# Optimization experiments

Hardware: AMD Instinct MI355X
Metric: run time of the kernel (lower is better)

The kernel has to match this reference:

```python
import jax, jax.numpy as jnp
import numpy as np

W, BHS, SEQ, H = 8, 2, 1024, 2048
FFN_PER = (4 * H) // W  # per-partition 4h width = 1024

def setup_inputs() -> dict:
    key = jax.random.key(0)
    k1, k2, k3 = jax.random.split(key, 3)
    # xavier-normal-ish scale for weights
    s1 = (2.0 / (H + FFN_PER)) ** 0.5
    s2 = (2.0 / (FFN_PER + H)) ** 0.5
    return {
        "hidden_states": jax.random.normal(k1, (W, BHS, SEQ, H), dtype=jnp.float32),
        "w1": jax.random.normal(k2, (W, H, FFN_PER), dtype=jnp.float32) * s1,
        "b1": jnp.zeros((W, 1, FFN_PER), dtype=jnp.float32),
        "w2": jax.random.normal(k3, (W, FFN_PER, H), dtype=jnp.float32) * s2,
        "b2": jnp.zeros((W, H), dtype=jnp.float32),
        "idx_list": jnp.arange(W, dtype=jnp.int64),
    }

def reference(hidden_states, w1, b1, w2, b2, idx_list):
    w, bhs, seq, h = hidden_states.shape
    # view [W, bhs, seq, h] -> [W, bhs*seq, h]
    x = hidden_states.reshape(w, bhs * seq, h)
    # column-parallel: baddbmm(bias, x, w1) -> [W, N, 4h/W]
    inter = jnp.einsum('wnh,whf->wnf', x, w1) + b1
    # exact (erf) gelu, matching torch F.gelu default
    inter = jax.nn.gelu(inter, approximate=False)
    # row-parallel: baddbmm(bias, inter, w2) -> [W, N, h]
    out_bias = b2[:, None, :]  # [W, 1, out]
    out = jnp.einsum('wnf,wfo->wno', inter, w2) + out_bias
    return (out, out_bias)
```

## Files before the change

### kernel.cpp

```cpp
#include <hip/hip_runtime.h>
#include <hip/hip_bf16.h>
#include <math.h>


typedef float f32x4 __attribute__((ext_vector_type(4)));
typedef short bf16x8 __attribute__((ext_vector_type(8)));
typedef short bf16x4 __attribute__((ext_vector_type(4)));
typedef unsigned short u16;

#define NW 8
#define MDIM 2048
#define HDIM 2048
#define FFN  1024

static __device__ __forceinline__ u16 f32_to_bf16_rn(float f) {
  union { float f; unsigned u; } v; v.f = f;
  unsigned r = v.u + 0x7FFF + ((v.u >> 16) & 1);
  return (u16)(r >> 16);
}

static __device__ __forceinline__ void gload_lds16(const void* g, void* l) {
  __builtin_amdgcn_global_load_lds(
      (const __attribute__((address_space(1))) void*)g,
      (__attribute__((address_space(3))) void*)l, 16, 0, 0);
}

__global__ void convert_bf16_kernel(const float* __restrict__ in,
                                    u16* __restrict__ out,
                                    const float* __restrict__ b2,
                                    float* __restrict__ outb) {
  int bid = blockIdx.x;
  if (bid >= NW * MDIM * HDIM / 4 / 256) {
    int i = (bid - NW * MDIM * HDIM / 4 / 256) * 256 + threadIdx.x;
    if (i < NW * HDIM) outb[i] = b2[i];
    return;
  }
  size_t i = (size_t)bid * blockDim.x + threadIdx.x;
  f32x4 v = ((const f32x4*)in)[i];
  bf16x4 p;
  p[0] = (short)f32_to_bf16_rn(v.x);
  p[1] = (short)f32_to_bf16_rn(v.y);
  p[2] = (short)f32_to_bf16_rn(v.z);
  p[3] = (short)f32_to_bf16_rn(v.w);
  ((bf16x4*)out)[i] = p;
}

__global__ void convert_transpose_kernel(const float* __restrict__ in,
                                         u16* __restrict__ out, int R, int C) {
  __shared__ u16 tile[64][68];
  int w = blockIdx.z;
  int c0 = blockIdx.x * 64, r0 = blockIdx.y * 64;
  int t = threadIdx.x;
  const float* ip = in + (size_t)w * R * C;
  u16* op = out + (size_t)w * C * R;
  int tr = t >> 4;
  int tc4 = (t & 15) * 4;
#pragma unroll
  for (int j = 0; j < 4; ++j) {
    int r = tr + j * 16;
    f32x4 v = *(const f32x4*)(ip + (size_t)(r0 + r) * C + c0 + tc4);
    tile[r][tc4 + 0] = f32_to_bf16_rn(v.x);
    tile[r][tc4 + 1] = f32_to_bf16_rn(v.y);
    tile[r][tc4 + 2] = f32_to_bf16_rn(v.z);
    tile[r][tc4 + 3] = f32_to_bf16_rn(v.w);
  }
  __syncthreads();
#pragma unroll
  for (int j = 0; j < 4; ++j) {
    int c = tr + j * 16;
    bf16x4 p;
    p[0] = (short)tile[tc4 + 0][c];
    p[1] = (short)tile[tc4 + 1][c];
    p[2] = (short)tile[tc4 + 2][c];
    p[3] = (short)tile[tc4 + 3][c];
    *(bf16x4*)(op + (size_t)(c0 + c) * R + r0 + tc4) = p;
  }
}

#define STAGE_AH(dst, tt, h)                                                  \
  do {                                                                        \
    gload_lds16(gA + (size_t)(h) * 128 * rowK + (size_t)(tt) * 128,           \
                (dst) + (h) * 16384 + tid * 16);                              \
    gload_lds16(gA + ((size_t)(h) * 128 + 64) * rowK + (size_t)(tt) * 128,    \
                (dst) + (h) * 16384 + 8192 + tid * 16);                       \
  } while (0)
#define STAGE_BH(dst, tt, h)                                                  \
  do {                                                                        \
    gload_lds16(gB + (size_t)(h) * 128 * rowK + (size_t)(tt) * 128,           \
                (dst) + 32768 + (h) * 16384 + tid * 16);                      \
    gload_lds16(gB + ((size_t)(h) * 128 + 64) * rowK + (size_t)(tt) * 128,    \
                (dst) + 32768 + (h) * 16384 + 8192 + tid * 16);               \
  } while (0)

#define LOAD_A(DST, SB, q)                                                    \
  _Pragma("unroll") for (int ii = 0; ii < 2; ++ii)                            \
      _Pragma("unroll") for (int kk = 0; kk < 2; ++kk)                        \
          DST[ii][kk] = *(const bf16x8*)((SB) + Aoff +                        \
              ((q)*32 + ii * 16 + ra) * 128 + (colsw ^ (kk << 6)))
#define LOAD_B(DST, SB)                                                       \
  _Pragma("unroll") for (int jj = 0; jj < 4; ++jj)                            \
      _Pragma("unroll") for (int kk = 0; kk < 2; ++kk)                        \
          DST[jj][kk] = *(const bf16x8*)((SB) + Boff +                        \
              (brow + jj * 16 + ra) * 128 + (colsw ^ (kk << 6)))

#define DO_PHASE(q, AF, BF, STAGES, VMCODE, PREFETCH)                         \
  {                                                                           \
    STAGES;                                                                   \
    __builtin_amdgcn_s_barrier();                                             \
    asm volatile("s_waitcnt lgkmcnt(0)" ::: "memory");                        \
    __builtin_amdgcn_sched_barrier(0);                                        \
    __builtin_amdgcn_s_setprio(1);                                            \
    _Pragma("unroll") for (int ii = 0; ii < 2; ++ii)                          \
        _Pragma("unroll") for (int jj = 0; jj < 4; ++jj)                      \
            _Pragma("unroll") for (int kk = 0; kk < 2; ++kk)                  \
                acc[(q)*2 + ii][jj] =                                         \
                    __builtin_amdgcn_mfma_f32_16x16x32_bf16(                  \
                        AF[ii][kk], BF[jj][kk], acc[(q)*2 + ii][jj],          \
                        0, 0, 0);                                             \
    __builtin_amdgcn_s_setprio(0);                                            \
    VMCODE;                                                                   \
    PREFETCH;                                                                 \
    __builtin_amdgcn_sched_barrier(0);                                        \
  }

template <bool GELU, bool C_F32>
__global__ __launch_bounds__(512, 2) void mlp_gemm(
    const u16* __restrict__ A, const u16* __restrict__ Bt,
    const float* __restrict__ bias, void* __restrict__ Cptr,
    int M, int N, int K, int nN) {
  __shared__ __align__(16) char lds[131072];
  char* cur = lds;
  char* nxt = lds + 65536;

  const int bid = blockIdx.x;
  const int w = bid & 7;
  const int jb = bid >> 3;
  const int m0 = (jb / nN) * 256;
  const int n0 = (jb % nN) * 256;

  const int tid = threadIdx.x;
  const int wid = tid >> 6, lane = tid & 63;
  const int wr = wid >> 2, wc = wid & 3;
  const int qa = lane >> 4, ra = lane & 15;

  const u16* ap = A + (size_t)w * M * K;
  const u16* btp = Bt + (size_t)w * N * K;
  const float* bp = bias + (size_t)w * N;

  const size_t rowK = (size_t)K * 2;
  const int r8 = tid >> 3;
  const int csw = ((tid & 7) * 16) ^ ((r8 & 7) << 4);
  const char* gA = (const char*)ap + (size_t)(m0 + r8) * rowK + csw;
  const char* gB = (const char*)btp + (size_t)(n0 + r8) * rowK + csw;

  const int colsw = (qa * 16) ^ ((ra & 7) << 4);
  const int Aoff = wr * 16384;
  const int Boff = 32768 + (wc >> 1) * 16384;
  const int brow = (wc & 1) * 64;

  f32x4 acc[8][4];
#pragma unroll
  for (int i = 0; i < 8; ++i)
#pragma unroll
    for (int j = 0; j < 4; ++j)
#pragma unroll
      for (int r = 0; r < 4; ++r) acc[i][j][r] = 0.0f;

  const int NT = K >> 6;
  const int nIter = NT >> 1;

  STAGE_BH(cur, 0, 0); STAGE_BH(cur, 0, 1);
  STAGE_AH(cur, 0, 0); STAGE_AH(cur, 0, 1);
  STAGE_BH(nxt, 1, 0); STAGE_BH(nxt, 1, 1);
  asm volatile("s_waitcnt vmcnt(4)" ::: "memory");
  __builtin_amdgcn_sched_barrier(0);
  __builtin_amdgcn_s_barrier();

  bf16x8 afrA[2][2], afrB[2][2], bfrA[4][2], bfrB[4][2];
  LOAD_B(bfrA, cur);
  LOAD_A(afrA, cur, 0);
  __builtin_amdgcn_sched_barrier(0);

  for (int it = 0; it < nIter; ++it) {
    const int t = it * 2;
    const bool s2 = (t + 2) < NT;

    DO_PHASE(0, afrA, bfrA, { STAGE_AH(nxt, t + 1, 0); }, {},
             { LOAD_A(afrB, cur, 1); });
    DO_PHASE(1, afrB, bfrA,
             { STAGE_AH(nxt, t + 1, 1); if (s2) STAGE_BH(cur, t + 2, 0); }, {},
             { LOAD_A(afrA, cur, 2); });
    DO_PHASE(2, afrA, bfrA, { if (s2) STAGE_BH(cur, t + 2, 1); }, {
      if (s2) asm volatile("s_waitcnt vmcnt(4)" ::: "memory");
      else    asm volatile("s_waitcnt vmcnt(0)" ::: "memory");
      __builtin_amdgcn_sched_barrier(0);
    }, { LOAD_A(afrB, cur, 3); });
    DO_PHASE(3, afrB, bfrA, {}, {},
             { LOAD_B(bfrB, nxt); LOAD_A(afrA, nxt, 0); });

    DO_PHASE(0, afrA, bfrB, { if (s2) STAGE_AH(cur, t + 2, 0); }, {},
             { LOAD_A(afrB, nxt, 1); });
    DO_PHASE(1, afrB, bfrB,
             { if (s2) { STAGE_AH(cur, t + 2, 1); STAGE_BH(nxt, t + 3, 0); } }, {},
             { LOAD_A(afrA, nxt, 2); });
    DO_PHASE(2, afrA, bfrB, { if (s2) STAGE_BH(nxt, t + 3, 1); }, {
      if (s2) asm volatile("s_waitcnt vmcnt(4)" ::: "memory");
      else    asm volatile("s_waitcnt vmcnt(0)" ::: "memory");
      __builtin_amdgcn_sched_barrier(0);
    }, { LOAD_A(afrB, nxt, 3); });
    DO_PHASE(3, afrB, bfrB, {}, {},
             { LOAD_B(bfrA, cur); LOAD_A(afrA, cur, 0); });
  }

#pragma unroll
  for (int i = 0; i < 8; ++i) {
#pragma unroll
    for (int j = 0; j < 4; ++j) {
      int col = n0 + wc * 64 + j * 16 + ra;
      float bv = bp[col];
#pragma unroll
      for (int r = 0; r < 4; ++r) {
        int row = m0 + wr * 128 + i * 16 + qa * 4 + r;
        float v = acc[i][j][r] + bv;
        if (GELU) v = 0.5f * v * (1.0f + erff(v * 0.70710678118654752f));
        if (C_F32)
          ((float*)Cptr)[(size_t)w * M * N + (size_t)row * N + col] = v;
        else
          ((u16*)Cptr)[(size_t)w * M * N + (size_t)row * N + col] =
              f32_to_bf16_rn(v);
      }
    }
  }
}

extern "C" void kernel_launch(void* const* d_in, const int* in_sizes, int n_in,
                              void* d_out, int out_size, void* d_ws,
                              size_t ws_size, hipStream_t stream) {
  const float* hs = (const float*)d_in[0];
  const float* w1 = (const float*)d_in[1];
  const float* b1 = (const float*)d_in[2];
  const float* w2 = (const float*)d_in[3];
  const float* b2 = (const float*)d_in[4];

  u16* W1t = (u16*)d_ws;
  u16* W2t = W1t + (size_t)NW * FFN * HDIM;
  u16* inter = W2t + (size_t)NW * HDIM * FFN;
  u16* XbWs = inter + (size_t)NW * MDIM * FFN;
  size_t need = ((size_t)NW * FFN * HDIM * 2 + (size_t)NW * MDIM * FFN +
                 (size_t)NW * MDIM * HDIM) * sizeof(u16);
  u16* Xb = (ws_size >= need) ? XbWs : (u16*)d_out;

  float* outb = (float*)d_out + (size_t)NW * MDIM * HDIM;

  convert_bf16_kernel<<<dim3(NW * MDIM * HDIM / 4 / 256 + 16), 256, 0,
                        stream>>>(hs, Xb, b2, outb);
  convert_transpose_kernel<<<dim3(FFN / 64, HDIM / 64, NW), 256, 0, stream>>>(
      w1, W1t, HDIM, FFN);
  convert_transpose_kernel<<<dim3(HDIM / 64, FFN / 64, NW), 256, 0, stream>>>(
      w2, W2t, FFN, HDIM);

  mlp_gemm<true, false>
      <<<dim3(NW * (MDIM / 256) * (FFN / 256)), 512, 0, stream>>>(
          Xb, W1t, b1, inter, MDIM, FFN, HDIM, FFN / 256);
  mlp_gemm<false, true>
      <<<dim3(NW * (MDIM / 256) * (HDIM / 256)), 512, 0, stream>>>(
          inter, W2t, b2, d_out, MDIM, HDIM, FFN, HDIM / 256);
}
```

Before: 237.2 us.

## Replace fine-grained phased pipeline with simple per-tile double-buffered loop

Swaps the hand-scheduled 8-phase main loop, which interleaved per-half A/B staging with barriers before every MFMA quarter, for a simpler loop. The new loop issues all next-tile global-to-LDS loads at the top, runs four MFMA quarters with register prefetch of A fragments, then does one vmcnt(0) wait and one barrier per K tile. The aim is fewer barriers and less scheduling overhead. In exchange the code waits for all outstanding loads each tile and gives up finer overlap of memory and compute. It also relies on a buffer swap without a barrier between reading cur and overwriting it next iteration, which the single barrier after the MFMAs covers.

```diff
diff --git a/kernel.cpp b/kernel.cpp
--- a/kernel.cpp
+++ b/kernel.cpp
@@ -103,24 +103,17 @@
           DST[jj][kk] = *(const bf16x8*)((SB) + Boff +                        \
               (brow + jj * 16 + ra) * 128 + (colsw ^ (kk << 6)))
 
-#define DO_PHASE(q, AF, BF, STAGES, VMCODE, PREFETCH)                         \
+#define MFMA_Q(q, AF)                                                         \
   {                                                                           \
-    STAGES;                                                                   \
-    __builtin_amdgcn_s_barrier();                                             \
-    asm volatile("s_waitcnt lgkmcnt(0)" ::: "memory");                        \
-    __builtin_amdgcn_sched_barrier(0);                                        \
     __builtin_amdgcn_s_setprio(1);                                            \
     _Pragma("unroll") for (int ii = 0; ii < 2; ++ii)                          \
         _Pragma("unroll") for (int jj = 0; jj < 4; ++jj)                      \
             _Pragma("unroll") for (int kk = 0; kk < 2; ++kk)                  \
                 acc[(q)*2 + ii][jj] =                                         \
                     __builtin_amdgcn_mfma_f32_16x16x32_bf16(                  \
-                        AF[ii][kk], BF[jj][kk], acc[(q)*2 + ii][jj],          \
+                        AF[ii][kk], bfr[jj][kk], acc[(q)*2 + ii][jj],         \
                         0, 0, 0);                                             \
     __builtin_amdgcn_s_setprio(0);                                            \
-    VMCODE;                                                                   \
-    PREFETCH;                                                                 \
-    __builtin_amdgcn_sched_barrier(0);                                        \
   }
 
 template <bool GELU, bool C_F32>
@@ -167,49 +160,42 @@
       for (int r = 0; r < 4; ++r) acc[i][j][r] = 0.0f;
 
   const int NT = K >> 6;
-  const int nIter = NT >> 1;
-
+
+  STAGE_AH(cur, 0, 0); STAGE_AH(cur, 0, 1);
   STAGE_BH(cur, 0, 0); STAGE_BH(cur, 0, 1);
-  STAGE_AH(cur, 0, 0); STAGE_AH(cur, 0, 1);
-  STAGE_BH(nxt, 1, 0); STAGE_BH(nxt, 1, 1);
-  asm volatile("s_waitcnt vmcnt(4)" ::: "memory");
+  asm volatile("s_waitcnt vmcnt(0)" ::: "memory");
+  __builtin_amdgcn_s_barrier();
   __builtin_amdgcn_sched_barrier(0);
-  __builtin_amdgcn_s_barrier();
-
-  bf16x8 afrA[2][2], afrB[2][2], bfrA[4][2], bfrB[4][2];
-  LOAD_B(bfrA, cur);
+
+  bf16x8 bfr[4][2], afrA[2][2], afrB[2][2];
+  LOAD_B(bfr, cur);
   LOAD_A(afrA, cur, 0);
-  __builtin_amdgcn_sched_barrier(0);
-
-  for (int it = 0; it < nIter; ++it) {
-    const int t = it * 2;
-    const bool s2 = (t + 2) < NT;
-
-    DO_PHASE(0, afrA, bfrA, { STAGE_AH(nxt, t + 1, 0); }, {},
-             { LOAD_A(afrB, cur, 1); });
-    DO_PHASE(1, afrB, bfrA,
-             { STAGE_AH(nxt, t + 1, 1); if (s2) STAGE_BH(cur, t + 2, 0); }, {},
-             { LOAD_A(afrA, cur, 2); });
-    DO_PHASE(2, afrA, bfrA, { if (s2) STAGE_BH(cur, t + 2, 1); }, {
-      if (s2) asm volatile("s_waitcnt vmcnt(4)" ::: "memory");
-      else    asm volatile("s_waitcnt vmcnt(0)" ::: "memory");
-      __builtin_amdgcn_sched_barrier(0);
-    }, { LOAD_A(afrB, cur, 3); });
-    DO_PHASE(3, afrB, bfrA, {}, {},
-             { LOAD_B(bfrB, nxt); LOAD_A(afrA, nxt, 0); });
-
-    DO_PHASE(0, afrA, bfrB, { if (s2) STAGE_AH(cur, t + 2, 0); }, {},
-             { LOAD_A(afrB, nxt, 1); });
-    DO_PHASE(1, afrB, bfrB,
-             { if (s2) { STAGE_AH(cur, t + 2, 1); STAGE_BH(nxt, t + 3, 0); } }, {},
-             { LOAD_A(afrA, nxt, 2); });
-    DO_PHASE(2, afrA, bfrB, { if (s2) STAGE_BH(nxt, t + 3, 1); }, {
-      if (s2) asm volatile("s_waitcnt vmcnt(4)" ::: "memory");
-      else    asm volatile("s_waitcnt vmcnt(0)" ::: "memory");
-      __builtin_amdgcn_sched_barrier(0);
-    }, { LOAD_A(afrB, nxt, 3); });
-    DO_PHASE(3, afrB, bfrB, {}, {},
-             { LOAD_B(bfrA, cur); LOAD_A(afrA, cur, 0); });
+
+  for (int t = 0; t < NT; ++t) {
+    const bool pf = (t + 1) < NT;
+    if (pf) {
+      STAGE_AH(nxt, t + 1, 0); STAGE_AH(nxt, t + 1, 1);
+      STAGE_BH(nxt, t + 1, 0); STAGE_BH(nxt, t + 1, 1);
+    }
+    __builtin_amdgcn_sched_barrier(0);
+
+    LOAD_A(afrB, cur, 1);
+    MFMA_Q(0, afrA);
+    LOAD_A(afrA, cur, 2);
+    MFMA_Q(1, afrB);
+    LOAD_A(afrB, cur, 3);
+    MFMA_Q(2, afrA);
+    MFMA_Q(3, afrB);
+
+    asm volatile("s_waitcnt vmcnt(0)" ::: "memory");
+    __builtin_amdgcn_s_barrier();
+    __builtin_amdgcn_sched_barrier(0);
+
+    if (pf) {
+      LOAD_B(bfr, nxt);
+      LOAD_A(afrA, nxt, 0);
+    }
+    char* tp = cur; cur = nxt; nxt = tp;
   }
 
 #pragma unroll
```

Result: no change. 233.6 us (-1.5%).
